# Performance work log

Hardware: AMD Instinct MI355X
Metric: run time of the kernel (lower is better)

## Reference

```python
import jax, jax.numpy as jnp
import numpy as np

N = 100000
E = 1250000
F_IN = 64
H = 64


def gcn_conv(x, W, b, src, dst, n):
    """PyG GCNConv: add self loops, symmetric D^-1/2 (A+I) D^-1/2 normalization."""
    h = x @ W  # [N, H]
    # degree after adding self-loops: 1 + in-degree at target nodes
    deg = 1.0 + jax.ops.segment_sum(jnp.ones((src.shape[0],), h.dtype), dst, num_segments=n)
    dinv = jax.lax.rsqrt(deg)  # deg >= 1, safe
    norm = dinv[src] * dinv[dst]  # [E]
    # neighbor aggregation (gather -> scale -> scatter-add) + self-loop term h[i]/deg[i]
    agg = jax.ops.segment_sum(h[src] * norm[:, None], dst, num_segments=n)
    return agg + h * (dinv * dinv)[:, None] + b


def setup_inputs() -> dict:
    key = jax.random.key(0)
    ks = jax.random.split(key, 8)
    x = jax.random.normal(ks[0], (N, F_IN), dtype=jnp.float32)
    edge_index = jax.random.randint(ks[1], (2, E), 0, N, dtype=jnp.int64 if jax.config.jax_enable_x64 else jnp.int32)
    s1 = 1.0 / np.sqrt(F_IN)
    s2 = 1.0 / np.sqrt(H)
    W1 = jax.random.uniform(ks[2], (F_IN, H), jnp.float32, -s1, s1)
    b1 = jnp.zeros((H,), jnp.float32)
    W2 = jax.random.uniform(ks[3], (H, H), jnp.float32, -s2, s2)
    b2 = jnp.zeros((H,), jnp.float32)
    Wo = jax.random.uniform(ks[4], (H, 1), jnp.float32, -s2, s2)
    bo = jax.random.uniform(ks[5], (1,), jnp.float32, -s2, s2)
    return {"x": x, "edge_index": edge_index, "W1": W1, "b1": b1, "W2": W2, "b2": b2, "Wo": Wo, "bo": bo}


def reference(x, edge_index, W1, b1, W2, b2, Wo, bo):
    src, dst = edge_index[0], edge_index[1]
    h = jax.nn.relu(gcn_conv(x, W1, b1, src, dst, N))
    h = jax.nn.relu(gcn_conv(h, W2, b2, src, dst, N))
    return h @ Wo + bo  # [N, 1]
```

## Files before the change

### kernel.cpp

```cpp
#include <hip/hip_runtime.h>


typedef float v2f __attribute__((ext_vector_type(2)));

constexpr int NB_SHIFT = 8;
constexpr int BUCK_NODES = 1 << NB_SHIFT;
constexpr int CAP = 5120;
constexpr int CHUNK = 4096;
constexpr int STPB = 512;

__global__ __launch_bounds__(512) void k_init(int* __restrict__ gcur, int nbuck,
                                              unsigned short* __restrict__ dummyRow) {
    int t = threadIdx.x;
    if (t < nbuck) gcur[t] = 0;
    if (t < 64) dummyRow[t] = 0;
}

__global__ __launch_bounds__(STPB) void k_bsort(const int* __restrict__ src,
                                                const int* __restrict__ dst, int E, int nbuck,
                                                int* __restrict__ gcur,
                                                unsigned* __restrict__ packed) {
    __shared__ int shStart[512];
    __shared__ int shCur[512];
    __shared__ int shOff[512];
    __shared__ unsigned stage[CHUNK];
    __shared__ unsigned short sbkt[CHUNK];
    const int tid = threadIdx.x;
    const int base = blockIdx.x * CHUNK;
    const int end = min(base + CHUNK, E);
    shCur[tid] = 0;
    __syncthreads();
    for (int e = base + tid; e < end; e += STPB)
        atomicAdd(&shCur[dst[e] >> NB_SHIFT], 1);
    __syncthreads();
    int v = shCur[tid];
    shStart[tid] = v;
    __syncthreads();
    for (int s = 1; s < 512; s <<= 1) {
        int a = (tid >= s) ? shStart[tid - s] : 0;
        __syncthreads();
        shStart[tid] += a;
        __syncthreads();
    }
    int exc = shStart[tid] - v;
    shStart[tid] = exc;
    shCur[tid] = exc;
    if (tid < nbuck) shOff[tid] = tid * CAP + ((v > 0) ? atomicAdd(&gcur[tid], v) : 0);
    __syncthreads();
    for (int e = base + tid; e < end; e += STPB) {
        int s = src[e];
        int d = dst[e];
        int b = d >> NB_SHIFT;
        int slot = atomicAdd(&shCur[b], 1);
        stage[slot] = ((unsigned)(d & (BUCK_NODES - 1)) << 17) | (unsigned)s;
        sbkt[slot] = (unsigned short)b;
    }
    __syncthreads();
    int cnt = end - base;
    for (int i = tid; i < cnt; i += STPB) {
        int b = sbkt[i];
        packed[shOff[b] + (i - shStart[b])] = stage[i];
    }
}

__global__ __launch_bounds__(512) void k_csr(const unsigned* __restrict__ packed,
                                             const int* __restrict__ gcur, int n,
                                             int* __restrict__ csr, int2* __restrict__ rowinfo,
                                             float* __restrict__ dinv) {
    __shared__ int cnt[BUCK_NODES];
    __shared__ int scn[BUCK_NODES];
    __shared__ int cur[BUCK_NODES];
    const int tid = threadIdx.x;
    const int e0 = blockIdx.x * CAP;
    const int e1 = e0 + gcur[blockIdx.x];
    if (tid < BUCK_NODES) cnt[tid] = 0;
    __syncthreads();
    for (int e = e0 + tid; e < e1; e += 512)
        atomicAdd(&cnt[packed[e] >> 17], 1);
    __syncthreads();
    int v = (tid < BUCK_NODES) ? cnt[tid] : 0;
    int pad = (v + 3) & ~3;
    if (tid < BUCK_NODES) scn[tid] = pad;
    __syncthreads();
    for (int s = 1; s < BUCK_NODES; s <<= 1) {
        int add = (tid >= s && tid < BUCK_NODES) ? scn[tid - s] : 0;
        __syncthreads();
        if (tid < BUCK_NODES) scn[tid] += add;
        __syncthreads();
    }
    int start = 0;
    if (tid < BUCK_NODES) {
        start = e0 + scn[tid] - pad;
        cur[tid] = start;
        int node = blockIdx.x * BUCK_NODES + tid;
        if (node < n) {
            rowinfo[node] = make_int2(start, pad);
            dinv[node] = rsqrtf(1.0f + (float)v);
        }
    }
    __syncthreads();
    for (int e = e0 + tid; e < e1; e += 512) {
        unsigned p = packed[e];
        int pos = atomicAdd(&cur[p >> 17], 1);
        csr[pos] = (int)(p & 0x1FFFFu);
    }
    __syncthreads();
    if (tid < BUCK_NODES) {
        for (int p = v; p < pad; ++p) csr[start + p] = n;
    }
}

__global__ __launch_bounds__(256) void k_gemm64bf(const float* __restrict__ A,
                                                  const float* __restrict__ W,
                                                  const float* __restrict__ dinv,
                                                  unsigned short* __restrict__ out,
                                                  int n) {
    const int lane = threadIdx.x & 63;
    const int wave = threadIdx.x >> 6;
    float wcol[64];
#pragma unroll
    for (int k = 0; k < 64; ++k) wcol[k] = W[k * 64 + lane];
    int base = blockIdx.x * 64;
    for (int r = wave; r < 64; r += 4) {
        int row = base + r;
        if (row >= n) break;
        float a = A[(size_t)row * 64 + lane];
        float acc = 0.0f;
#pragma unroll
        for (int k = 0; k < 64; ++k) {
            float ak = __uint_as_float(__builtin_amdgcn_readlane(__float_as_uint(a), k));
            acc = fmaf(ak, wcol[k], acc);
        }
        float val = acc * dinv[row];
        unsigned u = __float_as_uint(val);
        u = (u + 0x7FFFu + ((u >> 16) & 1u)) >> 16;
        out[(size_t)row * 64 + lane] = (unsigned short)u;
    }
}

__device__ __forceinline__ v2f bf2(unsigned u) {
    v2f r;
    r.x = __uint_as_float(u << 16);
    r.y = __uint_as_float(u & 0xFFFF0000u);
    return r;
}

template <bool LAST>
__global__ __launch_bounds__(256) void k_aggregate(
    const uint4* __restrict__ g4, const unsigned short* __restrict__ gRow,
    const int2* __restrict__ rowinfo, const int* __restrict__ csr,
    const float* __restrict__ dinv, const float* __restrict__ bias,
    const float* __restrict__ Wo, const float* __restrict__ bo,
    float* __restrict__ outRow, float* __restrict__ outHead, int n) {
    int w = (blockIdx.x * blockDim.x + threadIdx.x) >> 6;
    int lane = threadIdx.x & 63;
    const int h = lane >> 5;
    const int grp = (lane >> 3) & 3;
    const int q = lane & 7;
    int node = 2 * w + h;
    if (node >= n) return;
    int2 ri = rowinfo[node];
    const int e = ri.x;
    const int rnds = ri.y >> 2;
    int rm = max(rnds, __shfl_xor(rnds, 32, 64));
    v2f a0v = {0.f, 0.f}, a1v = {0.f, 0.f}, a2v = {0.f, 0.f}, a3v = {0.f, 0.f};
    int r = 0;
    for (; r + 2 <= rm; r += 2) {
        int c0 = csr[e + r * 4 + grp];
        int c1 = csr[e + r * 4 + 4 + grp];
        int i0 = (r < rnds) ? c0 : n;
        int i1 = (r + 1 < rnds) ? c1 : n;
        uint4 x0 = g4[(size_t)i0 * 8 + q];
        uint4 x1 = g4[(size_t)i1 * 8 + q];
        a0v += bf2(x0.x); a1v += bf2(x0.y); a2v += bf2(x0.z); a3v += bf2(x0.w);
        a0v += bf2(x1.x); a1v += bf2(x1.y); a2v += bf2(x1.z); a3v += bf2(x1.w);
    }
    if (r < rm) {
        int c0 = csr[e + r * 4 + grp];
        int i0 = (r < rnds) ? c0 : n;
        uint4 x0 = g4[(size_t)i0 * 8 + q];
        a0v += bf2(x0.x); a1v += bf2(x0.y); a2v += bf2(x0.z); a3v += bf2(x0.w);
    }
    bool g0 = (grp & 1) != 0;
    v2f keepA = g0 ? a2v : a0v;
    v2f keepB = g0 ? a3v : a1v;
    v2f sendA = g0 ? a0v : a2v;
    v2f sendB = g0 ? a1v : a3v;
    keepA.x += __shfl_xor(sendA.x, 8, 64);
    keepA.y += __shfl_xor(sendA.y, 8, 64);
    keepB.x += __shfl_xor(sendB.x, 8, 64);
    keepB.y += __shfl_xor(sendB.y, 8, 64);
    bool g1 = (grp & 2) != 0;
    v2f keep = g1 ? keepB : keepA;
    v2f send = g1 ? keepA : keepB;
    keep.x += __shfl_xor(send.x, 16, 64);
    keep.y += __shfl_xor(send.y, 16, 64);
    const int base = 8 * q + 4 * (grp & 1) + ((grp & 2) ? 2 : 0);
    unsigned su = *(const unsigned*)&gRow[(size_t)node * 64 + base];
    keep += bf2(su);
    float dv = dinv[node];
    float2 bb = *(const float2*)&bias[base];
    float ox = fmaxf(fmaf(dv, keep.x, bb.x), 0.f);
    float oy = fmaxf(fmaf(dv, keep.y, bb.y), 0.f);
    if constexpr (LAST) {
        float2 ww = *(const float2*)&Wo[base];
        float p = ox * ww.x + oy * ww.y;
#pragma unroll
        for (int m = 1; m <= 16; m <<= 1) p += __shfl_xor(p, m, 64);
        if ((lane & 31) == 0) outHead[node] = p + bo[0];
    } else {
        float2 o = make_float2(ox, oy);
        *(float2*)&outRow[(size_t)node * 64 + base] = o;
    }
}

extern "C" void kernel_launch(void* const* d_in, const int* in_sizes, int n_in,
                              void* d_out, int out_size, void* d_ws, size_t ws_size,
                              hipStream_t stream) {
    const float* x  = (const float*)d_in[0];
    const int*   ei = (const int*)d_in[1];
    const float* W1 = (const float*)d_in[2];
    const float* b1 = (const float*)d_in[3];
    const float* W2 = (const float*)d_in[4];
    const float* b2 = (const float*)d_in[5];
    const float* Wo = (const float*)d_in[6];
    const float* bo = (const float*)d_in[7];
    float* out = (float*)d_out;

    const int n = in_sizes[0] / 64;
    const int E = in_sizes[1] / 2;
    const int* src = ei;
    const int* dst = ei + E;

    const int nbuck = (n + BUCK_NODES - 1) >> NB_SHIFT;
    const int nchunks = (E + CHUNK - 1) / CHUNK;

    char* ws = (char*)d_ws;
    size_t off = 0;
    auto alloc = [&](size_t bytes) -> void* {
        void* p = ws + off;
        off += (bytes + 255) & ~(size_t)255;
        return p;
    };
    const size_t slabBytes = (size_t)nbuck * CAP * 4;
    const size_t hBytes    = (size_t)n * 64 * 4;
    const size_t gBytes    = (size_t)(n + 1) * 64 * 2;
    float*          dinv    = (float*)alloc((size_t)n * 4);
    int*            gcur    = (int*)alloc((size_t)nbuck * 4);
    int2*           rowinfo = (int2*)alloc((size_t)n * 8);
    int*            csr     = (int*)alloc(slabBytes);
    char*           regionA = (char*)alloc(hBytes > slabBytes ? hBytes : slabBytes);
    unsigned short* gBf     = (unsigned short*)alloc(gBytes);
    unsigned* packed = (unsigned*)regionA;
    float*    bufH   = (float*)regionA;

    k_init<<<1, 512, 0, stream>>>(gcur, nbuck, gBf + (size_t)n * 64);

    k_bsort<<<nchunks, STPB, 0, stream>>>(src, dst, E, nbuck, gcur, packed);
    k_csr<<<nbuck, 512, 0, stream>>>(packed, gcur, n, csr, rowinfo, dinv);

    const int gemmGrid = (n + 63) / 64;
    const int nodeGrid = (n + 7) / 8;

    k_gemm64bf<<<gemmGrid, 256, 0, stream>>>(x, W1, dinv, gBf, n);
    k_aggregate<false><<<nodeGrid, 256, 0, stream>>>((const uint4*)gBf, gBf, rowinfo, csr,
                                                     dinv, b1, nullptr, nullptr,
                                                     bufH, nullptr, n);
    k_gemm64bf<<<gemmGrid, 256, 0, stream>>>(bufH, W2, dinv, gBf, n);
    k_aggregate<true><<<nodeGrid, 256, 0, stream>>>((const uint4*)gBf, gBf, rowinfo, csr,
                                                    dinv, b2, Wo, bo,
                                                    nullptr, out, n);
}
```

Baseline: 158.1 us.

## Fold self-loop into CSR, aggregate four nodes per wave, use uniform row loads in GEMM

Each CSR row now gets its own node index as an extra entry, and rows are padded to a multiple of two instead of four. This removes the separate self-loop gather in the aggregation. The aggregation kernel maps four nodes per 64-lane wave, with 16 lanes per node, two neighbours per round and one shuffle stage. That lowers lane idling for low-degree nodes but gives each node fewer lanes and more rounds. The GEMM replaces per-k readlane broadcasts with wave-uniform row loads, which the compiler can turn into scalar loads.

```diff
diff --git a/kernel.cpp b/kernel.cpp
--- a/kernel.cpp
+++ b/kernel.cpp
@@ -79,7 +79,7 @@
         atomicAdd(&cnt[packed[e] >> 17], 1);
     __syncthreads();
     int v = (tid < BUCK_NODES) ? cnt[tid] : 0;
-    int pad = (v + 3) & ~3;
+    int pad = (v + 2) & ~1;
     if (tid < BUCK_NODES) scn[tid] = pad;
     __syncthreads();
     for (int s = 1; s < BUCK_NODES; s <<= 1) {
@@ -106,7 +106,9 @@
     }
     __syncthreads();
     if (tid < BUCK_NODES) {
-        for (int p = v; p < pad; ++p) csr[start + p] = n;
+        int node = blockIdx.x * BUCK_NODES + tid;
+        csr[start + v] = (node < n) ? node : n;
+        for (int p = v + 1; p < pad; ++p) csr[start + p] = n;
     }
 }
 
@@ -124,17 +126,15 @@
     for (int r = wave; r < 64; r += 4) {
         int row = base + r;
         if (row >= n) break;
-        float a = A[(size_t)row * 64 + lane];
+        int urow = __builtin_amdgcn_readfirstlane(row);
+        const float* Ar = A + (size_t)urow * 64;
         float acc = 0.0f;
 #pragma unroll
-        for (int k = 0; k < 64; ++k) {
-            float ak = __uint_as_float(__builtin_amdgcn_readlane(__float_as_uint(a), k));
-            acc = fmaf(ak, wcol[k], acc);
-        }
-        float val = acc * dinv[row];
+        for (int k = 0; k < 64; ++k) acc = fmaf(Ar[k], wcol[k], acc);
+        float val = acc * dinv[urow];
         unsigned u = __float_as_uint(val);
         u = (u + 0x7FFFu + ((u >> 16) & 1u)) >> 16;
-        out[(size_t)row * 64 + lane] = (unsigned short)u;
+        out[(size_t)urow * 64 + lane] = (unsigned short)u;
     }
 }
 
@@ -147,27 +147,29 @@
 
 template <bool LAST>
 __global__ __launch_bounds__(256) void k_aggregate(
-    const uint4* __restrict__ g4, const unsigned short* __restrict__ gRow,
+    const uint4* __restrict__ g4,
     const int2* __restrict__ rowinfo, const int* __restrict__ csr,
     const float* __restrict__ dinv, const float* __restrict__ bias,
     const float* __restrict__ Wo, const float* __restrict__ bo,
     float* __restrict__ outRow, float* __restrict__ outHead, int n) {
     int w = (blockIdx.x * blockDim.x + threadIdx.x) >> 6;
     int lane = threadIdx.x & 63;
-    const int h = lane >> 5;
-    const int grp = (lane >> 3) & 3;
+    const int s = lane >> 4;
+    const int grp = (lane >> 3) & 1;
     const int q = lane & 7;
-    int node = 2 * w + h;
-    if (node >= n) return;
-    int2 ri = rowinfo[node];
+    int node = 4 * w + s;
+    const bool valid = node < n;
+    int2 ri = valid ? rowinfo[node] : make_int2(0, 0);
     const int e = ri.x;
-    const int rnds = ri.y >> 2;
-    int rm = max(rnds, __shfl_xor(rnds, 32, 64));
+    const int rnds = ri.y >> 1;
+    int rm = rnds;
+    rm = max(rm, __shfl_xor(rm, 16, 64));
+    rm = max(rm, __shfl_xor(rm, 32, 64));
     v2f a0v = {0.f, 0.f}, a1v = {0.f, 0.f}, a2v = {0.f, 0.f}, a3v = {0.f, 0.f};
     int r = 0;
     for (; r + 2 <= rm; r += 2) {
-        int c0 = csr[e + r * 4 + grp];
-        int c1 = csr[e + r * 4 + 4 + grp];
+        int c0 = csr[e + 2 * r + grp];
+        int c1 = csr[e + 2 * r + 2 + grp];
         int i0 = (r < rnds) ? c0 : n;
         int i1 = (r + 1 < rnds) ? c1 : n;
         uint4 x0 = g4[(size_t)i0 * 8 + q];
@@ -176,41 +178,35 @@
         a0v += bf2(x1.x); a1v += bf2(x1.y); a2v += bf2(x1.z); a3v += bf2(x1.w);
     }
     if (r < rm) {
-        int c0 = csr[e + r * 4 + grp];
+        int c0 = csr[e + 2 * r + grp];
         int i0 = (r < rnds) ? c0 : n;
         uint4 x0 = g4[(size_t)i0 * 8 + q];
         a0v += bf2(x0.x); a1v += bf2(x0.y); a2v += bf2(x0.z); a3v += bf2(x0.w);
     }
-    bool g0 = (grp & 1) != 0;
-    v2f keepA = g0 ? a2v : a0v;
-    v2f keepB = g0 ? a3v : a1v;
-    v2f sendA = g0 ? a0v : a2v;
-    v2f sendB = g0 ? a1v : a3v;
-    keepA.x += __shfl_xor(sendA.x, 8, 64);
-    keepA.y += __shfl_xor(sendA.y, 8, 64);
-    keepB.x += __shfl_xor(sendB.x, 8, 64);
-    keepB.y += __shfl_xor(sendB.y, 8, 64);
-    bool g1 = (grp & 2) != 0;
-    v2f keep = g1 ? keepB : keepA;
-    v2f send = g1 ? keepA : keepB;
-    keep.x += __shfl_xor(send.x, 16, 64);
-    keep.y += __shfl_xor(send.y, 16, 64);
-    const int base = 8 * q + 4 * (grp & 1) + ((grp & 2) ? 2 : 0);
-    unsigned su = *(const unsigned*)&gRow[(size_t)node * 64 + base];
-    keep += bf2(su);
-    float dv = dinv[node];
-    float2 bb = *(const float2*)&bias[base];
-    float ox = fmaxf(fmaf(dv, keep.x, bb.x), 0.f);
-    float oy = fmaxf(fmaf(dv, keep.y, bb.y), 0.f);
+    v2f keep0 = grp ? a2v : a0v;
+    v2f keep1 = grp ? a3v : a1v;
+    v2f send0 = grp ? a0v : a2v;
+    v2f send1 = grp ? a1v : a3v;
+    keep0.x += __shfl_xor(send0.x, 8, 64);
+    keep0.y += __shfl_xor(send0.y, 8, 64);
+    keep1.x += __shfl_xor(send1.x, 8, 64);
+    keep1.y += __shfl_xor(send1.y, 8, 64);
+    const int base = 8 * q + 4 * grp;
+    float dv = valid ? dinv[node] : 0.f;
+    float4 bb = *(const float4*)&bias[base];
+    float4 vv;
+    vv.x = fmaxf(fmaf(dv, keep0.x, bb.x), 0.f);
+    vv.y = fmaxf(fmaf(dv, keep0.y, bb.y), 0.f);
+    vv.z = fmaxf(fmaf(dv, keep1.x, bb.z), 0.f);
+    vv.w = fmaxf(fmaf(dv, keep1.y, bb.w), 0.f);
     if constexpr (LAST) {
-        float2 ww = *(const float2*)&Wo[base];
-        float p = ox * ww.x + oy * ww.y;
+        float4 ww = *(const float4*)&Wo[base];
+        float p = vv.x * ww.x + vv.y * ww.y + vv.z * ww.z + vv.w * ww.w;
 #pragma unroll
-        for (int m = 1; m <= 16; m <<= 1) p += __shfl_xor(p, m, 64);
-        if ((lane & 31) == 0) outHead[node] = p + bo[0];
+        for (int m = 1; m <= 8; m <<= 1) p += __shfl_xor(p, m, 64);
+        if ((lane & 15) == 0 && valid) outHead[node] = p + bo[0];
     } else {
-        float2 o = make_float2(ox, oy);
-        *(float2*)&outRow[(size_t)node * 64 + base] = o;
+        if (valid) *(float4*)&outRow[(size_t)node * 64 + base] = vv;
     }
 }
 
@@ -260,14 +256,14 @@
     k_csr<<<nbuck, 512, 0, stream>>>(packed, gcur, n, csr, rowinfo, dinv);
 
     const int gemmGrid = (n + 63) / 64;
-    const int nodeGrid = (n + 7) / 8;
+    const int nodeGrid = (n + 15) / 16;
 
     k_gemm64bf<<<gemmGrid, 256, 0, stream>>>(x, W1, dinv, gBf, n);
-    k_aggregate<false><<<nodeGrid, 256, 0, stream>>>((const uint4*)gBf, gBf, rowinfo, csr,
+    k_aggregate<false><<<nodeGrid, 256, 0, stream>>>((const uint4*)gBf, rowinfo, csr,
                                                      dinv, b1, nullptr, nullptr,
                                                      bufH, nullptr, n);
     k_gemm64bf<<<gemmGrid, 256, 0, stream>>>(bufH, W2, dinv, gBf, n);
-    k_aggregate<true><<<nodeGrid, 256, 0, stream>>>((const uint4*)gBf, gBf, rowinfo, csr,
+    k_aggregate<true><<<nodeGrid, 256, 0, stream>>>((const uint4*)gBf, rowinfo, csr,
                                                     dinv, b2, Wo, bo,
                                                     nullptr, out, n);
 }
```

Result: faster. 140.4 us (median of 2 runs) (-11.2%).
